# Optimization experiments

Measured on AMD Instinct MI355X. Metric: run time of the kernel, lower is better.

## Reference

```python
import jax, jax.numpy as jnp
import numpy as np

NUM_HEADS = 16


def _layernorm(x, g, b, eps=1e-5):
    mu = x.mean(-1, keepdims=True)
    var = ((x - mu) ** 2).mean(-1, keepdims=True)
    return (x - mu) / jnp.sqrt(var + eps) * g + b


def _mha(q_in, kv, w_qkv, b_qkv, w_o, b_o, key_pad, num_heads):
    # Faithful nn.MultiheadAttention (batch_first, eval mode, same key/value).
    B, Lq, D = q_in.shape
    Lk = kv.shape[1]
    dh = D // num_heads
    wq, wk, wv = jnp.split(w_qkv, 3, axis=0)
    bq, bk, bv = jnp.split(b_qkv, 3, axis=0)
    q = (q_in @ wq.T + bq).reshape(B, Lq, num_heads, dh).transpose(0, 2, 1, 3)
    k = (kv @ wk.T + bk).reshape(B, Lk, num_heads, dh).transpose(0, 2, 1, 3)
    v = (kv @ wv.T + bv).reshape(B, Lk, num_heads, dh).transpose(0, 2, 1, 3)
    scores = jnp.einsum('bhqd,bhkd->bhqk', q, k) / jnp.sqrt(jnp.asarray(dh, q.dtype))
    scores = jnp.where(key_pad[:, None, None, :], -jnp.inf, scores)
    attn = jax.nn.softmax(scores, axis=-1)
    out = jnp.einsum('bhqk,bhkd->bhqd', attn, v).transpose(0, 2, 1, 3).reshape(B, Lq, D)
    return out @ w_o.T + b_o


def _forward(queries, text_feat, region_feat, text_mask, region_mask,
             w_qkv_t, b_qkv_t, w_o_t, b_o_t,
             w_qkv_r, b_qkv_r, w_o_r, b_o_r,
             ln_g, ln_b, w1, b1, w2, b2, alpha):
    kp_t = text_mask == 0
    kp_r = region_mask == 0
    q1 = _mha(queries, text_feat, w_qkv_t, b_qkv_t, w_o_t, b_o_t, kp_t, NUM_HEADS)
    q = _layernorm(queries + q1, ln_g, ln_b)
    q2 = _mha(q, region_feat, w_qkv_r, b_qkv_r, w_o_r, b_o_r, kp_r, NUM_HEADS)
    q = _layernorm(q + q2, ln_g, ln_b)
    # manual masked cross-attentions (note: scaled by sqrt(hidden_dim), not head_dim)
    scale = jnp.sqrt(jnp.asarray(q.shape[-1], q.dtype))
    at = jnp.einsum('bqd,btd->bqt', q, text_feat) / scale
    at = jnp.where(kp_t[:, None, :], -jnp.inf, at)
    agg_t = jax.nn.softmax(at, axis=-1) @ text_feat
    ar = jnp.einsum('bqd,brd->bqr', q, region_feat) / scale
    ar = jnp.where(kp_r[:, None, :], -jnp.inf, ar)
    agg_r = jax.nn.softmax(ar, axis=-1) @ region_feat
    q = q + alpha * agg_r + (1.0 - alpha) * agg_t
    # FFN: Linear(D,4D) -> GELU (exact) -> Linear(4D,D), dropout inactive (eval)
    h = jax.nn.gelu(q @ w1.T + b1, approximate=False)
    return q + (h @ w2.T + b2)


def setup_inputs() -> dict:
    B, NQ, LT, LR, D = 16, 128, 512, 196, 1024
    ks = jax.random.split(jax.random.key(0), 24)
    s = 0.02
    lens_t = jax.random.randint(ks[10], (B,), LT // 2, LT + 1)
    lens_r = jax.random.randint(ks[11], (B,), LR // 2, LR + 1)
    return {
        'queries': jax.random.normal(ks[0], (B, NQ, D), jnp.float32),
        'text_feat': jax.random.normal(ks[1], (B, LT, D), jnp.float32),
        'region_feat': jax.random.normal(ks[2], (B, LR, D), jnp.float32),
        'text_mask': (jnp.arange(LT)[None, :] < lens_t[:, None]).astype(jnp.int32),
        'region_mask': (jnp.arange(LR)[None, :] < lens_r[:, None]).astype(jnp.int32),
        'w_qkv_t': s * jax.random.normal(ks[3], (3 * D, D), jnp.float32),
        'b_qkv_t': jnp.zeros((3 * D,), jnp.float32),
        'w_o_t': s * jax.random.normal(ks[4], (D, D), jnp.float32),
        'b_o_t': jnp.zeros((D,), jnp.float32),
        'w_qkv_r': s * jax.random.normal(ks[5], (3 * D, D), jnp.float32),
        'b_qkv_r': jnp.zeros((3 * D,), jnp.float32),
        'w_o_r': s * jax.random.normal(ks[6], (D, D), jnp.float32),
        'b_o_r': jnp.zeros((D,), jnp.float32),
        'ln_g': jnp.ones((D,), jnp.float32),
        'ln_b': jnp.zeros((D,), jnp.float32),
        'w1': s * jax.random.normal(ks[7], (4 * D, D), jnp.float32),
        'b1': jnp.zeros((4 * D,), jnp.float32),
        'w2': s * jax.random.normal(ks[8], (D, 4 * D), jnp.float32),
        'b2': jnp.zeros((D,), jnp.float32),
        'alpha': jnp.asarray(0.5, jnp.float32),
    }


def reference(queries, text_feat, region_feat, text_mask, region_mask,
              w_qkv_t, b_qkv_t, w_o_t, b_o_t,
              w_qkv_r, b_qkv_r, w_o_r, b_o_r,
              ln_g, ln_b, w1, b1, w2, b2, alpha):
    return _forward(queries, text_feat, region_feat, text_mask, region_mask,
                    w_qkv_t, b_qkv_t, w_o_t, b_o_t,
                    w_qkv_r, b_qkv_r, w_o_r, b_o_r,
                    ln_g, ln_b, w1, b1, w2, b2, alpha)
```

## Files before the change

kernel.cpp:

```cpp
#include <hip/hip_runtime.h>
#include <hip/hip_bf16.h>


typedef __attribute__((ext_vector_type(8))) short short8;
typedef __attribute__((ext_vector_type(4))) float f32x4;

#define DEV static __device__ __forceinline__

DEV unsigned short f2bf(float f) {
    unsigned u = __float_as_uint(f);
    u += 0x7fffu + ((u >> 16) & 1u);
    return (unsigned short)(u >> 16);
}
DEV float bf2f(unsigned short u) {
    return __uint_as_float(((unsigned)u) << 16);
}

struct CvtPack {
    const float* src[9];
    unsigned short* dst[9];
    long start16[10];
};

__global__ __launch_bounds__(256)
void k_cvt_multi(CvtPack p, long total16) {
    long i = (long)blockIdx.x * blockDim.x + threadIdx.x;
    long stride = (long)gridDim.x * blockDim.x;
    for (; i < total16; i += stride) {
        int t = 0;
#pragma unroll
        for (int k = 1; k < 9; ++k) t += (i >= p.start16[k]) ? 1 : 0;
        long off = i - p.start16[t];
        const float4* s = (const float4*)p.src[t] + off * 4;
        float4 a = s[0], b = s[1], c = s[2], d = s[3];
        short8 o0, o1;
        o0[0] = (short)f2bf(a.x); o0[1] = (short)f2bf(a.y);
        o0[2] = (short)f2bf(a.z); o0[3] = (short)f2bf(a.w);
        o0[4] = (short)f2bf(b.x); o0[5] = (short)f2bf(b.y);
        o0[6] = (short)f2bf(b.z); o0[7] = (short)f2bf(b.w);
        o1[0] = (short)f2bf(c.x); o1[1] = (short)f2bf(c.y);
        o1[2] = (short)f2bf(c.z); o1[3] = (short)f2bf(c.w);
        o1[4] = (short)f2bf(d.x); o1[5] = (short)f2bf(d.y);
        o1[6] = (short)f2bf(d.z); o1[7] = (short)f2bf(d.w);
        short8* dp = (short8*)p.dst[t] + off * 2;
        dp[0] = o0;
        dp[1] = o1;
    }
}

__global__ __launch_bounds__(1024)
void k_gemm_nt256(const unsigned short* __restrict__ A, const unsigned short* __restrict__ B,
                  const float* __restrict__ bias,
                  float* __restrict__ outF, unsigned short* __restrict__ outB,
                  int M, int N, int K, int lda, int ldb, int ldc,
                  long sPart,
                  unsigned short* __restrict__ vT, int vColOff, long sVz, int vLd)
{
    __shared__ unsigned short smem[2 * 32768];

    unsigned gx = gridDim.x, gy = gridDim.y;
    unsigned nwg = gx * gy * gridDim.z;
    unsigned lin = (blockIdx.z * gy + blockIdx.y) * gx + blockIdx.x;
    unsigned bx = blockIdx.x, by = blockIdx.y, bz = blockIdx.z;
    if ((nwg & 7u) == 0u) {
        unsigned cpx = nwg >> 3;
        unsigned s = (lin & 7u) * cpx + (lin >> 3);
        bx = s % gx; unsigned r2 = s / gx;
        by = r2 % gy; bz = r2 / gy;
    }
    int s_k = (int)bz;
    const unsigned short* Ap = A + (long)s_k * K;
    const unsigned short* Bp = B + (long)s_k * K;
    float* outFp = outF ? outF + (long)s_k * sPart : nullptr;
    unsigned short* outBp = outB ? outB + (long)s_k * sPart : nullptr;

    int t = threadIdx.x;
    int wid = t >> 6, lane = t & 63;
    int lrow = lane & 15, kgrp = lane >> 4;
    int tm = by * 256, tn = bx * 256;
    int wm = (wid >> 2) * 64, wn = (wid & 3) * 64;

    auto stage = [&](int buf, int k0) {
#pragma unroll
        for (int r = 0; r < 2; ++r) {
            int d = r * 16384 + t * 16;
            int row = d >> 7;
            int colb = (d & 127) ^ ((row & 7) << 4);
            int gr = tm + row; if (gr > M - 1) gr = M - 1;
            const unsigned short* srcA = Ap + (long)gr * lda + k0 + (colb >> 1);
            unsigned short* dstA = smem + ((buf * 65536 + d) >> 1);
            __builtin_amdgcn_global_load_lds(
                (const __attribute__((address_space(1))) unsigned int*)srcA,
                (__attribute__((address_space(3))) unsigned int*)dstA, 16, 0, 0);
            int gn = tn + row; if (gn > N - 1) gn = N - 1;
            const unsigned short* srcB = Bp + (long)gn * ldb + k0 + (colb >> 1);
            unsigned short* dstB = smem + ((buf * 65536 + 32768 + d) >> 1);
            __builtin_amdgcn_global_load_lds(
                (const __attribute__((address_space(1))) unsigned int*)srcB,
                (__attribute__((address_space(3))) unsigned int*)dstB, 16, 0, 0);
        }
    };

    f32x4 acc[4][4] = {};
    int nt = K >> 6;

    stage(0, 0);

    for (int ti = 0; ti < nt; ++ti) {
        int cur = ti & 1;
        if (ti + 1 < nt) {
            stage(cur ^ 1, (ti + 1) << 6);
            asm volatile("s_waitcnt vmcnt(4)" ::: "memory");
        } else {
            asm volatile("s_waitcnt vmcnt(0)" ::: "memory");
        }
        __builtin_amdgcn_sched_barrier(0);
        __builtin_amdgcn_s_barrier();
        __builtin_amdgcn_sched_barrier(0);

        const char* Ab = (const char*)smem + cur * 65536;
        const char* Bb = Ab + 32768;
#pragma unroll
        for (int ks = 0; ks < 2; ++ks) {
            short8 a[4], bb[4];
            int kb = ks * 64 + kgrp * 16;
#pragma unroll
            for (int i = 0; i < 4; ++i) {
                int row = wm + i * 16 + lrow;
                a[i] = *(const short8*)(Ab + row * 128 + (kb ^ ((row & 7) << 4)));
            }
#pragma unroll
            for (int j = 0; j < 4; ++j) {
                int row = wn + j * 16 + lrow;
                bb[j] = *(const short8*)(Bb + row * 128 + (kb ^ ((row & 7) << 4)));
            }
#pragma unroll
            for (int i = 0; i < 4; ++i)
#pragma unroll
                for (int j = 0; j < 4; ++j)
                    acc[i][j] = __builtin_amdgcn_mfma_f32_16x16x32_bf16(a[i], bb[j], acc[i][j], 0, 0, 0);
        }
        __builtin_amdgcn_s_barrier();
    }

#pragma unroll
    for (int i = 0; i < 4; ++i) {
        int rbase = tm + wm + i * 16 + kgrp * 4;
#pragma unroll
        for (int j = 0; j < 4; ++j) {
            int c = tn + wn + j * 16 + lrow;
            if (c >= N) continue;
            float bv = bias ? bias[c] : 0.0f;
            float v[4];
#pragma unroll
            for (int e = 0; e < 4; ++e) v[e] = acc[i][j][e] + bv;
            if (vT && c >= vColOff) {
                if (rbase + 3 < M) {
                    int hh = (c - vColOff) >> 6, dd = (c - vColOff) & 63;
                    int bb2 = rbase >> 9, l = rbase & 511;
                    ushort4 o = { f2bf(v[0]), f2bf(v[1]), f2bf(v[2]), f2bf(v[3]) };
                    *(ushort4*)(vT + (long)(bb2 * 16 + hh) * sVz + (long)dd * vLd + l) = o;
                }
            } else {
#pragma unroll
                for (int e = 0; e < 4; ++e) {
                    int r = rbase + e;
                    if (r >= M) continue;
                    long oidx = (long)r * ldc + c;
                    if (outFp) outFp[oidx] = v[e];
                    if (outBp) outBp[oidx] = f2bf(v[e]);
                }
            }
        }
    }
}

__global__ __launch_bounds__(256)
void k_gemm_pv(const unsigned short* __restrict__ A, const unsigned short* __restrict__ B,
               unsigned short* __restrict__ outB,
               int K, int lda, int ldb, int ldc,
               int H, long sAb, long sAh, long sBz, long sCb, long sCh)
{
    __shared__ unsigned short smem[5 * 6144];

    int z = blockIdx.z;
    int b = z / H, h = z - b * H;
    const unsigned short* Ap = A + (long)b * sAb + (long)h * sAh;
    const unsigned short* Bp = B + (long)z * sBz;
    long offC = (long)b * sCb + (long)h * sCh;

    int t = threadIdx.x;
    int wid = t >> 6, lane = t & 63;
    int lrow = lane & 15, kgrp = lane >> 4;
    int wm = wid * 32;

    auto stage = [&](int buf, int k0) {
#pragma unroll
        for (int r = 0; r < 2; ++r) {
            int d = r * 4096 + t * 16;
            int row = d >> 6;
            int colb = (d & 63) ^ (((row >> 1) & 3) << 4);
            const unsigned short* srcA = Ap + (long)row * lda + k0 + (colb >> 1);
            unsigned short* dstA = smem + ((buf * 12288 + d) >> 1);
            __builtin_amdgcn_global_load_lds(
                (const __attribute__((address_space(1))) unsigned int*)srcA,
                (__attribute__((address_space(3))) unsigned int*)dstA, 16, 0, 0);
        }
        {
            int d = t * 16;
            int row = d >> 6;
            int colb = (d & 63) ^ (((row >> 1) & 3) << 4);
            const unsigned short* srcB = Bp + (long)row * ldb + k0 + (colb >> 1);
            unsigned short* dstB = smem + ((buf * 12288 + 8192 + d) >> 1);
            __builtin_amdgcn_global_load_lds(
                (const __attribute__((address_space(1))) unsigned int*)srcB,
                (__attribute__((address_space(3))) unsigned int*)dstB, 16, 0, 0);
        }
    };

    f32x4 acc[2][4] = {};
    int nt = K >> 5;

    for (int p = 0; p < 4 && p < nt; ++p) stage(p, p << 5);

    for (int ti = 0; ti < nt; ++ti) {
        int cur = ti % 5;
        int rem = nt - 1 - ti;
        if (rem >= 3)      asm volatile("s_waitcnt vmcnt(9)" ::: "memory");
        else if (rem == 2) asm volatile("s_waitcnt vmcnt(6)" ::: "memory");
        else if (rem == 1) asm volatile("s_waitcnt vmcnt(3)" ::: "memory");
        else               asm volatile("s_waitcnt vmcnt(0)" ::: "memory");
        __builtin_amdgcn_sched_barrier(0);
        __builtin_amdgcn_s_barrier();
        __builtin_amdgcn_sched_barrier(0);

        if (ti + 4 < nt) stage((ti + 4) % 5, (ti + 4) << 5);

        const char* Ab = (const char*)smem + cur * 12288;
        const char* Bb = Ab + 8192;
        short8 a[2], bb[4];
#pragma unroll
        for (int i = 0; i < 2; ++i) {
            int row = wm + i * 16 + lrow;
            a[i] = *(const short8*)(Ab + row * 64 + ((kgrp * 16) ^ (((row >> 1) & 3) << 4)));
        }
#pragma unroll
        for (int j = 0; j < 4; ++j) {
            int row = j * 16 + lrow;
            bb[j] = *(const short8*)(Bb + row * 64 + ((kgrp * 16) ^ (((row >> 1) & 3) << 4)));
        }
#pragma unroll
        for (int i = 0; i < 2; ++i)
#pragma unroll
            for (int j = 0; j < 4; ++j)
                acc[i][j] = __builtin_amdgcn_mfma_f32_16x16x32_bf16(a[i], bb[j], acc[i][j], 0, 0, 0);
    }

#pragma unroll
    for (int i = 0; i < 2; ++i) {
        int rbase = wm + i * 16 + kgrp * 4;
#pragma unroll
        for (int j = 0; j < 4; ++j) {
            int c = j * 16 + lrow;
#pragma unroll
            for (int e = 0; e < 4; ++e) {
                int r = rbase + e;
                outB[offC + (long)r * ldc + c] = f2bf(acc[i][j][e]);
            }
        }
    }
}

template<bool GELU>
__global__ __launch_bounds__(256)
void k_gemm_nt(const unsigned short* __restrict__ A, const unsigned short* __restrict__ B,
               const float* __restrict__ bias, const float* __restrict__ res,
               float* __restrict__ outF, unsigned short* __restrict__ outB,
               int M, int N, int K, int lda, int ldb, int ldc,
               int H, long sAb, long sAh, long sBb, long sBh, long sCb, long sCh,
               float scale, int S, long sPart,
               unsigned short* __restrict__ vT, int vColOff, long sVz, int vLd, int rpb)
{
    __shared__ unsigned short smem[5 * 8192];

    unsigned gx = gridDim.x, gy = gridDim.y, gz = gridDim.z;
    unsigned nwg = gx * gy * gz;
    unsigned lin = (blockIdx.z * gy + blockIdx.y) * gx + blockIdx.x;
    unsigned bx = blockIdx.x, by = blockIdx.y, bz = blockIdx.z;
    if ((nwg & 7u) == 0u) {
        unsigned cpx = nwg >> 3;
        unsigned s = (lin & 7u) * cpx + (lin >> 3);
        bx = s % gx; unsigned r2 = s / gx;
        by = r2 % gy; bz = r2 / gy;
    }

    int zz = (int)bz;
    int s_k = 0;
    if (S > 1) { s_k = zz % S; zz /= S; }
    int b = zz / H, h = zz - b * H;
    const unsigned short* Ap = A + (long)b * sAb + (long)h * sAh + (long)s_k * K;
    const unsigned short* Bp = B + (long)b * sBb + (long)h * sBh + (long)s_k * K;
    float* outFp = outF;
    if (outFp && S > 1) outFp += (long)s_k * sPart;
    unsigned short* outBp = outB;
    if (outBp && S > 1) outBp += (long)s_k * sPart;
    long offC = (long)b * sCb + (long)h * sCh;

    int t    = threadIdx.x;
    int wid  = t >> 6;
    int lane = t & 63;
    int lrow = lane & 15;
    int kgrp = lane >> 4;

    int tm = by * 128;
    int tn = bx * 128;
    int wm = (wid >> 1) * 64;
    int wn = (wid & 1) * 64;

    auto stage = [&](int buf, int k0) {
#pragma unroll
        for (int r = 0; r < 2; ++r) {
            int d = r * 4096 + t * 16;
            int row = d >> 6;
            int colb = (d & 63) ^ (((row >> 1) & 3) << 4);
            int gr = tm + row; if (gr > M - 1) gr = M - 1;
            const unsigned short* srcA = Ap + (long)gr * lda + k0 + (colb >> 1);
            unsigned short* dstA = smem + ((buf * 16384 + r * 4096 + wid * 1024) >> 1);
            __builtin_amdgcn_global_load_lds(
                (const __attribute__((address_space(1))) unsigned int*)srcA,
                (__attribute__((address_space(3))) unsigned int*)dstA, 16, 0, 0);
            int gn = tn + row; if (gn > N - 1) gn = N - 1;
            const unsigned short* srcB = Bp + (long)gn * ldb + k0 + (colb >> 1);
            unsigned short* dstB = smem + ((buf * 16384 + 8192 + r * 4096 + wid * 1024) >> 1);
            __builtin_amdgcn_global_load_lds(
                (const __attribute__((address_space(1))) unsigned int*)srcB,
                (__attribute__((address_space(3))) unsigned int*)dstB, 16, 0, 0);
        }
    };

    f32x4 acc[4][4] = {};
    int nt = K >> 5;

    for (int p = 0; p < 4 && p < nt; ++p) stage(p, p << 5);

    for (int ti = 0; ti < nt; ++ti) {
        int cur = ti % 5;
        int rem = nt - 1 - ti;
        if (rem >= 3)      asm volatile("s_waitcnt vmcnt(12)" ::: "memory");
        else if (rem == 2) asm volatile("s_waitcnt vmcnt(8)"  ::: "memory");
        else if (rem == 1) asm volatile("s_waitcnt vmcnt(4)"  ::: "memory");
        else               asm volatile("s_waitcnt vmcnt(0)"  ::: "memory");
        __builtin_amdgcn_sched_barrier(0);
        __builtin_amdgcn_s_barrier();
        __builtin_amdgcn_sched_barrier(0);

        if (ti + 4 < nt) stage((ti + 4) % 5, (ti + 4) << 5);

        const char* Ab = (const char*)smem + cur * 16384;
        const char* Bb = Ab + 8192;
        short8 a[4], bb[4];
#pragma unroll
        for (int i = 0; i < 4; ++i) {
            int row = wm + i * 16 + lrow;
            a[i] = *(const short8*)(Ab + row * 64 + ((kgrp * 16) ^ (((row >> 1) & 3) << 4)));
        }
#pragma unroll
        for (int j = 0; j < 4; ++j) {
            int row = wn + j * 16 + lrow;
            bb[j] = *(const short8*)(Bb + row * 64 + ((kgrp * 16) ^ (((row >> 1) & 3) << 4)));
        }
#pragma unroll
        for (int i = 0; i < 4; ++i)
#pragma unroll
            for (int j = 0; j < 4; ++j)
                acc[i][j] = __builtin_amdgcn_mfma_f32_16x16x32_bf16(a[i], bb[j], acc[i][j], 0, 0, 0);
    }

#pragma unroll
    for (int i = 0; i < 4; ++i) {
        int rbase = tm + wm + i * 16 + kgrp * 4;
#pragma unroll
        for (int j = 0; j < 4; ++j) {
            int c = tn + wn + j * 16 + lrow;
            if (c >= N) continue;
            float bv = bias ? bias[c] : 0.0f;
            if (vT && c >= vColOff) {
                int hh = (c - vColOff) >> 6, dd = (c - vColOff) & 63;
#pragma unroll
                for (int e = 0; e < 4; ++e) {
                    int r = rbase + e;
                    if (r >= M) continue;
                    float v = acc[i][j][e] * scale + bv;
                    int bb2 = r / rpb, l = r - bb2 * rpb;
                    vT[(long)(bb2 * 16 + hh) * sVz + (long)dd * vLd + l] = f2bf(v);
                }
                continue;
            }
#pragma unroll
            for (int e = 0; e < 4; ++e) {
                int r = rbase + e;
                if (r >= M) continue;
                float v = acc[i][j][e] * scale + bv;
                long oidx = offC + (long)r * ldc + c;
                if (res) v += res[oidx];
                if (GELU) v = 0.5f * v * (1.0f + erff(v * 0.70710678118654752f));
                if (outFp) outFp[oidx] = v;
                if (outBp) outBp[oidx] = f2bf(v);
            }
        }
    }
}

__global__ __launch_bounds__(256)
void k_redux_b(const unsigned short* __restrict__ part, long sPart, int S,
               const float* __restrict__ bias, const float* __restrict__ res,
               float* __restrict__ outF, unsigned short* __restrict__ outB,
               long n8, int ldc8, int gelu)
{
    long i = (long)blockIdx.x * blockDim.x + threadIdx.x;
    long stride = (long)gridDim.x * blockDim.x;
    for (; i < n8; i += stride) {
        long e0 = i * 8;
        float v[8];
        short8 p0 = *(const short8*)(part + e0);
#pragma unroll
        for (int k = 0; k < 8; ++k) v[k] = bf2f((unsigned short)p0[k]);
        for (int s = 1; s < S; ++s) {
            short8 ps = *(const short8*)(part + e0 + (long)s * sPart);
#pragma unroll
            for (int k = 0; k < 8; ++k) v[k] += bf2f((unsigned short)ps[k]);
        }
        if (bias) {
            int c = (int)(i % ldc8) * 8;
            float4 b0 = *(const float4*)(bias + c);
            float4 b1 = *(const float4*)(bias + c + 4);
            v[0] += b0.x; v[1] += b0.y; v[2] += b0.z; v[3] += b0.w;
            v[4] += b1.x; v[5] += b1.y; v[6] += b1.z; v[7] += b1.w;
        }
        if (res) {
            float4 r0 = *(const float4*)(res + e0);
            float4 r1 = *(const float4*)(res + e0 + 4);
            v[0] += r0.x; v[1] += r0.y; v[2] += r0.z; v[3] += r0.w;
            v[4] += r1.x; v[5] += r1.y; v[6] += r1.z; v[7] += r1.w;
        }
        if (gelu) {
#pragma unroll
            for (int k = 0; k < 8; ++k)
                v[k] = 0.5f * v[k] * (1.0f + erff(v[k] * 0.70710678118654752f));
        }
        if (outF) {
            float4 o0 = { v[0], v[1], v[2], v[3] };
            float4 o1 = { v[4], v[5], v[6], v[7] };
            *(float4*)(outF + e0) = o0;
            *(float4*)(outF + e0 + 4) = o1;
        }
        if (outB) {
            short8 o;
#pragma unroll
            for (int k = 0; k < 8; ++k) o[k] = (short)f2bf(v[k]);
            *(short8*)(outB + e0) = o;
        }
    }
}

__global__ __launch_bounds__(256)
void k_redux_ln_b(const unsigned short* __restrict__ part, long sPart, int S,
                  const float* __restrict__ bias, const float* __restrict__ res,
                  const float* __restrict__ g, const float* __restrict__ bt,
                  float* __restrict__ yf, unsigned short* __restrict__ yb)
{
    int row = blockIdx.x;
    int t = threadIdx.x;
    int lane = t & 63, wid = t >> 6;
    long base = (long)row * 1024 + t * 4;

    ushort4 p0 = *(const ushort4*)(part + base);
    float v0 = bf2f(p0.x), v1 = bf2f(p0.y), v2 = bf2f(p0.z), v3 = bf2f(p0.w);
    for (int s = 1; s < S; ++s) {
        ushort4 ps = *(const ushort4*)(part + base + (long)s * sPart);
        v0 += bf2f(ps.x); v1 += bf2f(ps.y); v2 += bf2f(ps.z); v3 += bf2f(ps.w);
    }
    float4 bv = *(const float4*)(bias + t * 4);
    v0 += bv.x; v1 += bv.y; v2 += bv.z; v3 += bv.w;
    float4 rv = *(const float4*)(res + base);
    v0 += rv.x; v1 += rv.y; v2 += rv.z; v3 += rv.w;

    float s1 = v0 + v1 + v2 + v3;
    float s2 = v0 * v0 + v1 * v1 + v2 * v2 + v3 * v3;
#pragma unroll
    for (int d = 32; d > 0; d >>= 1) { s1 += __shfl_xor(s1, d, 64); s2 += __shfl_xor(s2, d, 64); }
    __shared__ float rs[4], rss[4];
    if (lane == 0) { rs[wid] = s1; rss[wid] = s2; }
    __syncthreads();
    s1 = rs[0] + rs[1] + rs[2] + rs[3];
    s2 = rss[0] + rss[1] + rss[2] + rss[3];
    float mu  = s1 * (1.0f / 1024.0f);
    float var = s2 * (1.0f / 1024.0f) - mu * mu;
    float inv = rsqrtf(var + 1e-5f);

    float4 gv = *(const float4*)(g + t * 4);
    float4 btv = *(const float4*)(bt + t * 4);
    float o0 = (v0 - mu) * inv * gv.x + btv.x;
    float o1 = (v1 - mu) * inv * gv.y + btv.y;
    float o2 = (v2 - mu) * inv * gv.z + btv.z;
    float o3 = (v3 - mu) * inv * gv.w + btv.w;
    float4 of = { o0, o1, o2, o3 };
    ushort4 ob = { f2bf(o0), f2bf(o1), f2bf(o2), f2bf(o3) };
    *(float4*)(yf + base) = of;
    *(ushort4*)(yb + base) = ob;
}

__global__ __launch_bounds__(256)
void k_tr(const unsigned short* __restrict__ in, unsigned short* __restrict__ out,
          int R, int ldin, int ldout,
          int H, long sIb, long sIh, long sOz)
{
    __shared__ unsigned short tile[32][33];
    int z = blockIdx.z;
    int b = z / H, h = z - b * H;
    const unsigned short* ip = in + (long)b * sIb + (long)h * sIh;
    unsigned short* op = out + (long)z * sOz;
    int t = threadIdx.x;
    int cl = t & 31, rl = t >> 5;
    int c0 = blockIdx.x * 32, r0 = blockIdx.y * 32;
#pragma unroll
    for (int i = 0; i < 4; ++i) {
        int r = r0 + rl + i * 8;
        unsigned short v = 0;
        if (r < R) v = ip[(long)r * ldin + (c0 + cl)];
        tile[rl + i * 8][cl] = v;
    }
    __syncthreads();
#pragma unroll
    for (int i = 0; i < 4; ++i) {
        int orow = c0 + rl + i * 8;
        int ocol = r0 + cl;
        op[(long)orow * ldout + ocol] = tile[cl][rl + i * 8];
    }
}

__global__ __launch_bounds__(256)
void k_softmax_w(const float* __restrict__ sc, long sPart, int S,
                 unsigned short* __restrict__ P,
                 const int* __restrict__ mask, int L, int Lpad,
                 int ld_sc, int ld_p, int rows_per_batch, int nrows)
{
    int gw = (int)((blockIdx.x * 256 + threadIdx.x) >> 6);
    if (gw >= nrows) return;
    int lane = threadIdx.x & 63;
    int b = gw / rows_per_batch;
    const float* p = sc + (long)gw * ld_sc;
    unsigned short* po = P + (long)gw * ld_p;
    const int* mrow = mask + (long)b * L;

    int nch = (Lpad + 255) >> 8;
    float v[2][4];
    float mx = -INFINITY;
#pragma unroll
    for (int c = 0; c < 2; ++c) {
        if (c >= nch) { v[c][0]=v[c][1]=v[c][2]=v[c][3] = -INFINITY; continue; }
        int j = c * 256 + lane * 4;
        if (j < L) {
            float4 x = *(const float4*)(p + j);
            for (int s = 1; s < S; ++s) {
                float4 y = *(const float4*)(p + j + (long)s * sPart);
                x.x += y.x; x.y += y.y; x.z += y.z; x.w += y.w;
            }
            int4 m = *(const int4*)(mrow + j);
            v[c][0] = m.x ? x.x : -INFINITY;
            v[c][1] = m.y ? x.y : -INFINITY;
            v[c][2] = m.z ? x.z : -INFINITY;
            v[c][3] = m.w ? x.w : -INFINITY;
        } else {
            v[c][0]=v[c][1]=v[c][2]=v[c][3] = -INFINITY;
        }
        mx = fmaxf(mx, fmaxf(fmaxf(v[c][0], v[c][1]), fmaxf(v[c][2], v[c][3])));
    }
#pragma unroll
    for (int d = 32; d > 0; d >>= 1) mx = fmaxf(mx, __shfl_xor(mx, d, 64));

    float sum = 0.f;
#pragma unroll
    for (int c = 0; c < 2; ++c)
#pragma unroll
        for (int k = 0; k < 4; ++k) {
            float e = (v[c][k] == -INFINITY) ? 0.0f : __expf(v[c][k] - mx);
            v[c][k] = e;
            sum += e;
        }
#pragma unroll
    for (int d = 32; d > 0; d >>= 1) sum += __shfl_xor(sum, d, 64);
    float inv = 1.0f / sum;

#pragma unroll
    for (int c = 0; c < 2; ++c) {
        if (c >= nch) continue;
        int j = c * 256 + lane * 4;
        if (j < Lpad) {
            ushort4 o;
            o.x = f2bf(v[c][0] * inv);
            o.y = f2bf(v[c][1] * inv);
            o.z = f2bf(v[c][2] * inv);
            o.w = f2bf(v[c][3] * inv);
            *(ushort4*)(po + j) = o;
        }
    }
}

__global__ void k_combine_b(float* __restrict__ qf, unsigned short* __restrict__ qb,
                            const unsigned short* __restrict__ aggtp,
                            const unsigned short* __restrict__ aggrp,
                            const float* __restrict__ alpha, long n4, long sPart, int S)
{
    float a = *alpha;
    long i = (long)blockIdx.x * blockDim.x + threadIdx.x;
    long stride = (long)gridDim.x * blockDim.x;
    for (; i < n4; i += stride) {
        long e0 = i * 4;
        float st[4] = {0.f, 0.f, 0.f, 0.f}, sr[4] = {0.f, 0.f, 0.f, 0.f};
        for (int s = 0; s < S; ++s) {
            ushort4 pt = *(const ushort4*)(aggtp + e0 + (long)s * sPart);
            ushort4 pr = *(const ushort4*)(aggrp + e0 + (long)s * sPart);
            st[0] += bf2f(pt.x); st[1] += bf2f(pt.y); st[2] += bf2f(pt.z); st[3] += bf2f(pt.w);
            sr[0] += bf2f(pr.x); sr[1] += bf2f(pr.y); sr[2] += bf2f(pr.z); sr[3] += bf2f(pr.w);
        }
        float4 q = *(const float4*)(qf + e0);
        float v0 = q.x + a * sr[0] + (1.0f - a) * st[0];
        float v1 = q.y + a * sr[1] + (1.0f - a) * st[1];
        float v2 = q.z + a * sr[2] + (1.0f - a) * st[2];
        float v3 = q.w + a * sr[3] + (1.0f - a) * st[3];
        float4 of = { v0, v1, v2, v3 };
        ushort4 ob = { f2bf(v0), f2bf(v1), f2bf(v2), f2bf(v3) };
        *(float4*)(qf + e0) = of;
        *(ushort4*)(qb + e0) = ob;
    }
}

extern "C" void kernel_launch(void* const* d_in, const int* in_sizes, int n_in,
                              void* d_out, int out_size, void* d_ws, size_t ws_size,
                              hipStream_t stream)
{
    const float* queries = (const float*)d_in[0];
    const float* text    = (const float*)d_in[1];
    const float* region  = (const float*)d_in[2];
    const int*   tmask   = (const int*)d_in[3];
    const int*   rmask   = (const int*)d_in[4];
    const float* w_qkv_t = (const float*)d_in[5];
    const float* b_qkv_t = (const float*)d_in[6];
    const float* w_o_t   = (const float*)d_in[7];
    const float* b_o_t   = (const float*)d_in[8];
    const float* w_qkv_r = (const float*)d_in[9];
    const float* b_qkv_r = (const float*)d_in[10];
    const float* w_o_r   = (const float*)d_in[11];
    const float* b_o_r   = (const float*)d_in[12];
    const float* ln_g    = (const float*)d_in[13];
    const float* ln_b    = (const float*)d_in[14];
    const float* w1      = (const float*)d_in[15];
    const float* b1      = (const float*)d_in[16];
    const float* w2      = (const float*)d_in[17];
    const float* b2      = (const float*)d_in[18];
    const float* alpha   = (const float*)d_in[19];

    const int Bn = 16, NQ = 128, LT = 512, LR = 196, D = 1024, H = 16;
    const int LRp = 256;
    const int MQ = Bn * NQ;
    const int MT = Bn * LT;
    const int MR = Bn * LR;

    char* ws = (char*)d_ws;
    size_t off = 0;
    auto alloc = [&](size_t bytes) -> void* {
        void* p = ws + off;
        off = (off + bytes + 255) & ~(size_t)255;
        return p;
    };
    unsigned short* qb     = (unsigned short*)alloc((size_t)MQ * D * 2);
    unsigned short* tb     = (unsigned short*)alloc((size_t)MT * D * 2);
    unsigned short* rb     = (unsigned short*)alloc((size_t)MR * D * 2);
    unsigned short* wqkvtb = (unsigned short*)alloc((size_t)3 * D * D * 2);
    unsigned short* wotb   = (unsigned short*)alloc((size_t)D * D * 2);
    unsigned short* wqkvrb = (unsigned short*)alloc((size_t)3 * D * D * 2);
    unsigned short* worb   = (unsigned short*)alloc((size_t)D * D * 2);
    unsigned short* w1b    = (unsigned short*)alloc((size_t)4 * D * D * 2);
    unsigned short* w2b    = (unsigned short*)alloc((size_t)4 * D * D * 2);
    unsigned short* ktv    = (unsigned short*)alloc((size_t)MT * 2 * D * 2);
    unsigned short* krv    = (unsigned short*)alloc((size_t)MR * 2 * D * 2);
    unsigned short* vtT    = (unsigned short*)alloc((size_t)Bn * H * 64 * LT * 2);
    unsigned short* vrT    = (unsigned short*)alloc((size_t)Bn * H * 64 * LRp * 2);
    unsigned short* qp     = (unsigned short*)alloc((size_t)MQ * D * 2);
    unsigned short* ao     = (unsigned short*)alloc((size_t)MQ * D * 2);
    unsigned short* qlnb   = (unsigned short*)alloc((size_t)MQ * D * 2);
    float* qlf  = (float*)alloc((size_t)MQ * D * 4);
    float* sc   = (float*)alloc((size_t)Bn * H * NQ * LT * 4);
    if (off > ws_size) return;

    unsigned short* tbT = ktv;
    unsigned short* rbT = ktv + (size_t)Bn * D * LT;
    float* sct = sc;
    float* scr = sc;
    unsigned short* Pt = (unsigned short*)sc;
    unsigned short* Pr = (unsigned short*)(sc + 1 * 1048576);
    float* atp   = sc + 2 * 1048576;
    float* arp   = sc + 6 * 1048576;
    unsigned short* aggtp_b = (unsigned short*)((char*)sc + (size_t)32 * 1048576);
    unsigned short* aggrp_b = (unsigned short*)((char*)sc + (size_t)48 * 1048576);
    unsigned short* hb = (unsigned short*)sc;
    unsigned short* part_qb  = (unsigned short*)sc;
    unsigned short* part_f1b = ktv;
    unsigned short* part_f2b = ktv;

    const long PQ = (long)MQ * D;

    {
        CvtPack pk;
        const float* srcs[9] = { queries, text, region, w_qkv_t, w_o_t, w_qkv_r, w_o_r, w1, w2 };
        unsigned short* dsts[9] = { qb, tb, rb, wqkvtb, wotb, wqkvrb, worb, w1b, w2b };
        long ns[9] = { (long)MQ * D, (long)MT * D, (long)MR * D, (long)3 * D * D,
                       (long)D * D, (long)3 * D * D, (long)D * D, (long)4 * D * D,
                       (long)4 * D * D };
        long acc16 = 0;
        pk.start16[0] = 0;
        for (int i = 0; i < 9; ++i) {
            pk.src[i] = srcs[i]; pk.dst[i] = dsts[i];
            acc16 += ns[i] / 16;
            pk.start16[i + 1] = acc16;
        }
        k_cvt_multi<<<2048, 256, 0, stream>>>(pk, acc16);
    }

    auto NT = [&](const unsigned short* A, const unsigned short* Bm, const float* bias,
                  const float* res, float* oF, unsigned short* oB,
                  int M, int N, int K, int lda, int ldb, int ldc,
                  int Hh, long sAb, long sAh, long sBb, long sBh, long sCb, long sCh,
                  int batch, float scale, bool gelu, int S = 1, long sPart = 0,
                  unsigned short* vT = nullptr, int vColOff = 0, long sVz = 0,
                  int vLd = 0, int rpb = 1) {
        dim3 g((N + 127) / 128, (M + 127) / 128, batch * S);
        if (gelu)
            k_gemm_nt<true><<<g, 256, 0, stream>>>(A, Bm, bias, res, oF, oB, M, N, K,
                lda, ldb, ldc, Hh, sAb, sAh, sBb, sBh, sCb, sCh, scale, S, sPart,
                vT, vColOff, sVz, vLd, rpb);
        else
            k_gemm_nt<false><<<g, 256, 0, stream>>>(A, Bm, bias, res, oF, oB, M, N, K,
                lda, ldb, ldc, Hh, sAb, sAh, sBb, sBh, sCb, sCh, scale, S, sPart,
                vT, vColOff, sVz, vLd, rpb);
    };
    auto NT256 = [&](const unsigned short* A, const unsigned short* Bm, const float* bias,
                     float* oF, unsigned short* oB, int M, int N, int Kc,
                     int lda, int ldb, int ldc, int S, long sPart,
                     unsigned short* vT = nullptr, int vColOff = 0, long sVz = 0,
                     int vLd = 0) {
        dim3 g((N + 255) / 256, (M + 255) / 256, S);
        k_gemm_nt256<<<g, 1024, 0, stream>>>(A, Bm, bias, oF, oB, M, N, Kc,
                                             lda, ldb, ldc, sPart, vT, vColOff, sVz, vLd);
    };
    auto REDUXB = [&](const unsigned short* part, long sPart, int S, const float* bias,
                      const float* res, float* oF, unsigned short* oB,
                      long total, int ldc, int gelu) {
        long n8 = total / 8;
        int blocks = (int)((n8 + 255) / 256);
        if (blocks > 2048) blocks = 2048;
        k_redux_b<<<blocks, 256, 0, stream>>>(part, sPart, S, bias, res, oF, oB,
                                              n8, ldc / 8, gelu);
    };
    auto SMAX = [&](const float* scp, long sPart, int S, unsigned short* P,
                    const int* mask, int L, int Lpad, int ld_sc, int ld_p,
                    int rpb, int nrows) {
        int blocks = (nrows + 3) / 4;
        k_softmax_w<<<blocks, 256, 0, stream>>>(scp, sPart, S, P, mask, L, Lpad,
                                                ld_sc, ld_p, rpb, nrows);
    };

    NT256(tb, wqkvtb + (long)D * D, b_qkv_t + D, nullptr, ktv,
          MT, 2 * D, D, D, D, 2 * D, 1, 0,
          vtT, D, (long)64 * LT, LT);
    NT(rb, wqkvrb + (long)D * D, b_qkv_r + D, nullptr, nullptr, krv,
       MR, 2 * D, D, D, D, 2 * D, 1,0,0,0,0,0,0, 1, 1.0f, false, 1, 0,
       vrT, D, (long)64 * LRp, LRp, LR);

    NT(qb, wqkvtb, nullptr, nullptr, nullptr, part_qb, MQ, D, 512, D, D, D,
       1,0,0,0,0,0,0, 1, 1.0f, false, 2, PQ);
    REDUXB(part_qb, PQ, 2, b_qkv_t, nullptr, nullptr, qp, PQ, D, 0);
    NT(qp, ktv, nullptr, nullptr, sct, nullptr, NQ, LT, 64, D, 2 * D, LT,
       H, (long)NQ * D, 64, (long)LT * 2 * D, 64, (long)H * NQ * LT, (long)NQ * LT,
       Bn * H, 0.125f, false);
    SMAX(sct, 0, 1, (unsigned short*)sct, tmask, LT, LT, LT, 2 * LT,
         H * NQ, Bn * H * NQ);
    k_gemm_pv<<<dim3(1, 1, Bn * H), 256, 0, stream>>>(
        (const unsigned short*)sct, vtT, ao, LT, 2 * LT, LT, D,
        H, (long)H * NQ * 2 * LT, (long)NQ * 2 * LT, (long)64 * LT,
        (long)NQ * D, 64);
    NT(ao, wotb, nullptr, nullptr, nullptr, part_qb, MQ, D, 512, D, D, D,
       1,0,0,0,0,0,0, 1, 1.0f, false, 2, PQ);
    k_redux_ln_b<<<MQ, 256, 0, stream>>>(part_qb, PQ, 2, b_o_t, queries,
                                         ln_g, ln_b, qlf, qlnb);

    NT(qlnb, wqkvrb, nullptr, nullptr, nullptr, part_qb, MQ, D, 512, D, D, D,
       1,0,0,0,0,0,0, 1, 1.0f, false, 2, PQ);
    REDUXB(part_qb, PQ, 2, b_qkv_r, nullptr, nullptr, qp, PQ, D, 0);
    NT(qp, krv, nullptr, nullptr, scr, nullptr, NQ, LR, 64, D, 2 * D, LRp,
       H, (long)NQ * D, 64, (long)LR * 2 * D, 64, (long)H * NQ * LRp, (long)NQ * LRp,
       Bn * H, 0.125f, false);
    SMAX(scr, 0, 1, (unsigned short*)scr, rmask, LR, LRp, LRp, 2 * LRp,
         H * NQ, Bn * H * NQ);
    k_gemm_pv<<<dim3(1, 1, Bn * H), 256, 0, stream>>>(
        (const unsigned short*)scr, vrT, ao, LRp, 2 * LRp, LRp, D,
        H, (long)H * NQ * 2 * LRp, (long)NQ * 2 * LRp, (long)64 * LRp,
        (long)NQ * D, 64);
    NT(ao, worb, nullptr, nullptr, nullptr, part_qb, MQ, D, 512, D, D, D,
       1,0,0,0,0,0,0, 1, 1.0f, false, 2, PQ);
    k_redux_ln_b<<<MQ, 256, 0, stream>>>(part_qb, PQ, 2, b_o_r, qlf,
                                         ln_g, ln_b, qlf, qlnb);

    {
        dim3 g1(D / 32, LT / 32, Bn);
        k_tr<<<g1, 256, 0, stream>>>(tb, tbT, LT, D, LT, 1, (long)LT * D, 0, (long)D * LT);
        dim3 g2(D / 32, LRp / 32, Bn);
        k_tr<<<g2, 256, 0, stream>>>(rb, rbT, LR, D, LRp, 1, (long)LR * D, 0, (long)D * LRp);
    }
    NT(qlnb, tb, nullptr, nullptr, atp, nullptr, NQ, LT, 256, D, D, LT,
       1, (long)NQ * D, 0, (long)LT * D, 0, (long)NQ * LT, 0, Bn, 0.03125f, false,
       4, (long)Bn * NQ * LT);
    SMAX(atp, (long)Bn * NQ * LT, 4, Pt, tmask, LT, LT, LT, LT, NQ, Bn * NQ);
    NT(Pt, tbT, nullptr, nullptr, nullptr, aggtp_b, NQ, D, 256, LT, LT, D,
       1, (long)NQ * LT, 0, (long)D * LT, 0, (long)NQ * D, 0, Bn, 1.0f, false,
       2, PQ);
    NT(qlnb, rb, nullptr, nullptr, arp, nullptr, NQ, LR, 256, D, D, LRp,
       1, (long)NQ * D, 0, (long)LR * D, 0, (long)NQ * LRp, 0, Bn, 0.03125f, false,
       4, (long)Bn * NQ * LRp);
    SMAX(arp, (long)Bn * NQ * LRp, 4, Pr, rmask, LR, LRp, LRp, LRp, NQ, Bn * NQ);
    NT(Pr, rbT, nullptr, nullptr, nullptr, aggrp_b, NQ, D, 128, LRp, LRp, D,
       1, (long)NQ * LRp, 0, (long)D * LRp, 0, (long)NQ * D, 0, Bn, 1.0f, false,
       2, PQ);

    k_combine_b<<<2048, 256, 0, stream>>>(qlf, qlnb, aggtp_b, aggrp_b, alpha,
                                          (long)MQ * D / 4, PQ, 2);

    NT256(qlnb, w1b, nullptr, nullptr, part_f1b, MQ, 4 * D, 512,
          D, D, 4 * D, 2, (long)MQ * 4 * D);
    REDUXB(part_f1b, (long)MQ * 4 * D, 2, b1, nullptr, nullptr, hb,
           (long)MQ * 4 * D, 4 * D, 1);
    NT256(hb, w2b, nullptr, nullptr, part_f2b, MQ, D, 512,
          4 * D, 4 * D, D, 8, PQ);
    REDUXB(part_f2b, PQ, 8, b2, qlf, (float*)d_out, nullptr, PQ, D, 0);
}
```

Measured before the change: 489.5 us.

## Generalize PV kernel into tiled 128x64 GEMM and drop split-K reductions

The per-head PV kernel becomes a general 128x64-tile GEMM with an XCD-aware block remap and a fused bias/residual epilogue. The Q projections, output projections and FFN second layer now use it without split-K, which removes the separate partial-sum reduction kernels and their memory traffic. The cost is fewer parallel blocks per GEMM and a longer K loop per block, which may underutilize the GPU for small M.

```diff
diff --git a/kernel.cpp b/kernel.cpp
--- a/kernel.cpp
+++ b/kernel.cpp
@@ -176,14 +176,26 @@
 }
 
 __global__ __launch_bounds__(256)
-void k_gemm_pv(const unsigned short* __restrict__ A, const unsigned short* __restrict__ B,
-               unsigned short* __restrict__ outB,
-               int K, int lda, int ldb, int ldc,
-               int H, long sAb, long sAh, long sBz, long sCb, long sCh)
+void k_gemm_n64(const unsigned short* __restrict__ A, const unsigned short* __restrict__ B,
+                const float* __restrict__ bias, const float* __restrict__ res,
+                float* __restrict__ outF, unsigned short* __restrict__ outB,
+                int K, int lda, int ldb, int ldc,
+                int H, long sAb, long sAh, long sBz, long sCb, long sCh)
 {
     __shared__ unsigned short smem[5 * 6144];
 
-    int z = blockIdx.z;
+    unsigned gx = gridDim.x, gy = gridDim.y;
+    unsigned nwg = gx * gy * gridDim.z;
+    unsigned lin = (blockIdx.z * gy + blockIdx.y) * gx + blockIdx.x;
+    unsigned bx = blockIdx.x, by = blockIdx.y, bz = blockIdx.z;
+    if ((nwg & 7u) == 0u) {
+        unsigned cpx = nwg >> 3;
+        unsigned s = (lin & 7u) * cpx + (lin >> 3);
+        bx = s % gx; unsigned r2 = s / gx;
+        by = r2 % gy; bz = r2 / gy;
+    }
+
+    int z = (int)bz;
     int b = z / H, h = z - b * H;
     const unsigned short* Ap = A + (long)b * sAb + (long)h * sAh;
     const unsigned short* Bp = B + (long)z * sBz;
@@ -192,6 +204,7 @@
     int t = threadIdx.x;
     int wid = t >> 6, lane = t & 63;
     int lrow = lane & 15, kgrp = lane >> 4;
+    int tm = by * 128, tn = bx * 64;
     int wm = wid * 32;
 
     auto stage = [&](int buf, int k0) {
@@ -200,7 +213,7 @@
             int d = r * 4096 + t * 16;
             int row = d >> 6;
             int colb = (d & 63) ^ (((row >> 1) & 3) << 4);
-            const unsigned short* srcA = Ap + (long)row * lda + k0 + (colb >> 1);
+            const unsigned short* srcA = Ap + (long)(tm + row) * lda + k0 + (colb >> 1);
             unsigned short* dstA = smem + ((buf * 12288 + d) >> 1);
             __builtin_amdgcn_global_load_lds(
                 (const __attribute__((address_space(1))) unsigned int*)srcA,
@@ -210,7 +223,7 @@
             int d = t * 16;
             int row = d >> 6;
             int colb = (d & 63) ^ (((row >> 1) & 3) << 4);
-            const unsigned short* srcB = Bp + (long)row * ldb + k0 + (colb >> 1);
+            const unsigned short* srcB = Bp + (long)(tn + row) * ldb + k0 + (colb >> 1);
             unsigned short* dstB = smem + ((buf * 12288 + 8192 + d) >> 1);
             __builtin_amdgcn_global_load_lds(
                 (const __attribute__((address_space(1))) unsigned int*)srcB,
@@ -258,14 +271,19 @@
 
 #pragma unroll
     for (int i = 0; i < 2; ++i) {
-        int rbase = wm + i * 16 + kgrp * 4;
+        int rbase = tm + wm + i * 16 + kgrp * 4;
 #pragma unroll
         for (int j = 0; j < 4; ++j) {
-            int c = j * 16 + lrow;
+            int c = tn + j * 16 + lrow;
+            float bv = bias ? bias[c] : 0.0f;
 #pragma unroll
             for (int e = 0; e < 4; ++e) {
                 int r = rbase + e;
-                outB[offC + (long)r * ldc + c] = f2bf(acc[i][j][e]);
+                long oidx = offC + (long)r * ldc + c;
+                float v = acc[i][j][e] + bv;
+                if (res) v += res[oidx];
+                if (outF) outF[oidx] = v;
+                if (outB) outB[oidx] = f2bf(v);
             }
         }
     }
@@ -707,7 +725,6 @@
     unsigned short* hb = (unsigned short*)sc;
     unsigned short* part_qb  = (unsigned short*)sc;
     unsigned short* part_f1b = ktv;
-    unsigned short* part_f2b = ktv;
 
     const long PQ = (long)MQ * D;
 
@@ -754,6 +771,14 @@
         k_gemm_nt256<<<g, 1024, 0, stream>>>(A, Bm, bias, oF, oB, M, N, Kc,
                                              lda, ldb, ldc, sPart, vT, vColOff, sVz, vLd);
     };
+    auto N64 = [&](const unsigned short* A, const unsigned short* Bm, const float* bias,
+                   const float* res, float* oF, unsigned short* oB,
+                   int M, int N, int K, int lda, int ldb, int ldc,
+                   int Hh, long sAb, long sAh, long sBz, long sCb, long sCh, int Z) {
+        dim3 g(N / 64, M / 128, Z);
+        k_gemm_n64<<<g, 256, 0, stream>>>(A, Bm, bias, res, oF, oB, K,
+                                          lda, ldb, ldc, Hh, sAb, sAh, sBz, sCb, sCh);
+    };
     auto REDUXB = [&](const unsigned short* part, long sPart, int S, const float* bias,
                       const float* res, float* oF, unsigned short* oB,
                       long total, int ldc, int gelu) {
@@ -778,38 +803,36 @@
        MR, 2 * D, D, D, D, 2 * D, 1,0,0,0,0,0,0, 1, 1.0f, false, 1, 0,
        vrT, D, (long)64 * LRp, LRp, LR);
 
-    NT(qb, wqkvtb, nullptr, nullptr, nullptr, part_qb, MQ, D, 512, D, D, D,
-       1,0,0,0,0,0,0, 1, 1.0f, false, 2, PQ);
-    REDUXB(part_qb, PQ, 2, b_qkv_t, nullptr, nullptr, qp, PQ, D, 0);
+    N64(qb, wqkvtb, b_qkv_t, nullptr, nullptr, qp, MQ, D, D, D, D, D,
+        1, 0, 0, 0, 0, 0, 1);
     NT(qp, ktv, nullptr, nullptr, sct, nullptr, NQ, LT, 64, D, 2 * D, LT,
        H, (long)NQ * D, 64, (long)LT * 2 * D, 64, (long)H * NQ * LT, (long)NQ * LT,
        Bn * H, 0.125f, false);
     SMAX(sct, 0, 1, (unsigned short*)sct, tmask, LT, LT, LT, 2 * LT,
          H * NQ, Bn * H * NQ);
-    k_gemm_pv<<<dim3(1, 1, Bn * H), 256, 0, stream>>>(
-        (const unsigned short*)sct, vtT, ao, LT, 2 * LT, LT, D,
+    N64((const unsigned short*)sct, vtT, nullptr, nullptr, nullptr, ao,
+        NQ, 64, LT, 2 * LT, LT, D,
         H, (long)H * NQ * 2 * LT, (long)NQ * 2 * LT, (long)64 * LT,
-        (long)NQ * D, 64);
-    NT(ao, wotb, nullptr, nullptr, nullptr, part_qb, MQ, D, 512, D, D, D,
-       1,0,0,0,0,0,0, 1, 1.0f, false, 2, PQ);
-    k_redux_ln_b<<<MQ, 256, 0, stream>>>(part_qb, PQ, 2, b_o_t, queries,
+        (long)NQ * D, 64, Bn * H);
+    N64(ao, wotb, nullptr, nullptr, nullptr, part_qb, MQ, D, D, D, D, D,
+        1, 0, 0, 0, 0, 0, 1);
+    k_redux_ln_b<<<MQ, 256, 0, stream>>>(part_qb, PQ, 1, b_o_t, queries,
                                          ln_g, ln_b, qlf, qlnb);
 
-    NT(qlnb, wqkvrb, nullptr, nullptr, nullptr, part_qb, MQ, D, 512, D, D, D,
-       1,0,0,0,0,0,0, 1, 1.0f, false, 2, PQ);
-    REDUXB(part_qb, PQ, 2, b_qkv_r, nullptr, nullptr, qp, PQ, D, 0);
+    N64(qlnb, wqkvrb, b_qkv_r, nullptr, nullptr, qp, MQ, D, D, D, D, D,
+        1, 0, 0, 0, 0, 0, 1);
     NT(qp, krv, nullptr, nullptr, scr, nullptr, NQ, LR, 64, D, 2 * D, LRp,
        H, (long)NQ * D, 64, (long)LR * 2 * D, 64, (long)H * NQ * LRp, (long)NQ * LRp,
        Bn * H, 0.125f, false);
     SMAX(scr, 0, 1, (unsigned short*)scr, rmask, LR, LRp, LRp, 2 * LRp,
          H * NQ, Bn * H * NQ);
-    k_gemm_pv<<<dim3(1, 1, Bn * H), 256, 0, stream>>>(
-        (const unsigned short*)scr, vrT, ao, LRp, 2 * LRp, LRp, D,
+    N64((const unsigned short*)scr, vrT, nullptr, nullptr, nullptr, ao,
+        NQ, 64, LRp, 2 * LRp, LRp, D,
         H, (long)H * NQ * 2 * LRp, (long)NQ * 2 * LRp, (long)64 * LRp,
-        (long)NQ * D, 64);
-    NT(ao, worb, nullptr, nullptr, nullptr, part_qb, MQ, D, 512, D, D, D,
-       1,0,0,0,0,0,0, 1, 1.0f, false, 2, PQ);
-    k_redux_ln_b<<<MQ, 256, 0, stream>>>(part_qb, PQ, 2, b_o_r, qlf,
+        (long)NQ * D, 64, Bn * H);
+    N64(ao, worb, nullptr, nullptr, nullptr, part_qb, MQ, D, D, D, D, D,
+        1, 0, 0, 0, 0, 0, 1);
+    k_redux_ln_b<<<MQ, 256, 0, stream>>>(part_qb, PQ, 1, b_o_r, qlf,
                                          ln_g, ln_b, qlf, qlnb);
 
     {
@@ -840,7 +863,6 @@
           D, D, 4 * D, 2, (long)MQ * 4 * D);
     REDUXB(part_f1b, (long)MQ * 4 * D, 2, b1, nullptr, nullptr, hb,
            (long)MQ * 4 * D, 4 * D, 1);
-    NT256(hb, w2b, nullptr, nullptr, part_f2b, MQ, D, 512,
-          4 * D, 4 * D, D, 8, PQ);
-    REDUXB(part_f2b, PQ, 8, b2, qlf, (float*)d_out, nullptr, PQ, D, 0);
-}
+    N64(hb, w2b, b2, qlf, (float*)d_out, nullptr, MQ, D, 4 * D, 4 * D, 4 * D, D,
+        1, 0, 0, 0, 0, 0, 1);
+}
```

Result: faster. 467.5 us (-4.5%).
